# Kernel tuning notes

Measured on AMD Instinct MI355X. Metric: run time of the kernel, lower is better.

Reference implementation:

```python
import jax, jax.numpy as jnp
import numpy as np

N_HEADS = 8
FACTOR = 5


def setup_inputs() -> dict:
    key = jax.random.key(0)
    ks = jax.random.split(key, 8)
    B, L, D = 2, 4096, 512
    sample_k = min(FACTOR * int(np.ceil(np.log(L))), L)  # 45
    inp = {
        "queries": jax.random.normal(ks[0], (B, L, D), jnp.float32),
        "keys": jax.random.normal(ks[1], (B, L, D), jnp.float32),
        "values": jax.random.normal(ks[2], (B, L, D), jnp.float32),
        "Wq": jax.random.normal(ks[3], (D, D), jnp.float32) * 0.02,
        "bq": jnp.zeros((D,), jnp.float32),
        "Wk": jax.random.normal(ks[4], (D, D), jnp.float32) * 0.02,
        "bk": jnp.zeros((D,), jnp.float32),
        "Wv": jax.random.normal(ks[5], (D, D), jnp.float32) * 0.02,
        "bv": jnp.zeros((D,), jnp.float32),
        "index_sample": jax.random.randint(ks[6], (L, sample_k), 0, L, jnp.int32),
    }
    return inp


def reference(queries, keys, values, Wq, bq, Wk, bk, Wv, bv, index_sample):
    b, l_q, d_model = queries.shape
    _, l_k, _ = keys.shape
    h = N_HEADS
    d = d_model // h
    # projections -> [b, h, l, d]
    q = (queries @ Wq + bq).reshape(b, l_q, h, d).transpose(0, 2, 1, 3)
    k = (keys @ Wk + bk).reshape(b, l_k, h, d).transpose(0, 2, 1, 3)
    v = (values @ Wv + bv).reshape(b, l_k, h, d).transpose(0, 2, 1, 3)
    n_top = min(FACTOR * int(np.ceil(np.log(l_q))), l_q)
    # --- prob_qk: sparse sampled QK ---
    # gather sampled keys per query position: [b, h, l_q, sample_k, d]
    k_sample = k[:, :, index_sample, :]
    q_k_sample = jnp.einsum('bhld,bhlsd->bhls', q, k_sample)
    # sparsity measure M(q, K) = max - mean
    m = q_k_sample.max(-1) - q_k_sample.sum(-1) / l_k  # [b, h, l_q]
    _, m_top = jax.lax.top_k(m, n_top)  # [b, h, n_top]
    q_reduce = jnp.take_along_axis(q, m_top[..., None], axis=2)  # [b, h, u, d]
    scores = jnp.einsum('bhud,bhkd->bhuk', q_reduce, k)  # [b, h, u, l_k]
    scale = float(1.0 / np.sqrt(d))
    scores = scores * scale
    # --- causal ProbMask on the selected query rows ---
    causal = jnp.triu(jnp.ones((l_q, l_k), bool), 1)
    mask = causal[m_top]  # [b, h, u, l_k]
    scores = jnp.where(mask, -jnp.inf, scores)
    attn = jax.nn.softmax(scores, axis=-1)
    # --- initial context: causal cumsum of V; scatter updated rows ---
    context = jnp.cumsum(v, axis=2)  # [b, h, l_q, d]
    upd = jnp.einsum('bhuk,bhkd->bhud', attn, v)
    bi = jnp.arange(b)[:, None, None]
    hi = jnp.arange(h)[None, :, None]
    context = context.at[bi, hi, m_top].set(upd)
    return context.transpose(0, 2, 1, 3).reshape(b, l_q, h * d)
```

## Files before the change

kernel.cpp:

```cpp
#include <hip/hip_runtime.h>
#include <math.h>

#define B  2
#define L  4096
#define D  512
#define H  8
#define DH 64
#define BH (B * H)
#define K3 1536
#define XPW 1024

typedef short s16x8 __attribute__((ext_vector_type(8)));
typedef float f32x4 __attribute__((ext_vector_type(4)));

#define AS1 __attribute__((address_space(1)))
#define AS3 __attribute__((address_space(3)))

__device__ __forceinline__ void lds_load16(const void* g, void* l) {
    __builtin_amdgcn_global_load_lds((const AS1 unsigned int*)g,
                                     (AS3 unsigned int*)l, 16, 0, 0);
}

__device__ __forceinline__ unsigned short f2bf(float x) {
    union { float f; unsigned u; } v; v.f = x;
    unsigned u = v.u;
    return (unsigned short)((u + 0x7fff + ((u >> 16) & 1)) >> 16);
}
__device__ __forceinline__ float bf2f(unsigned short h) {
    union { float f; unsigned u; } v; v.u = ((unsigned)h) << 16;
    return v.f;
}

#define MEMFENCE asm volatile("" ::: "memory")
__device__ __forceinline__ void wg_bar() {
    MEMFENCE;
    __builtin_amdgcn_s_barrier();
    MEMFENCE;
}

__global__ __launch_bounds__(256)
void k_split(const float* __restrict__ q, const float* __restrict__ k,
             const float* __restrict__ v,
             const float* __restrict__ wq, const float* __restrict__ wk,
             const float* __restrict__ wv,
             unsigned short* __restrict__ Xp, unsigned short* __restrict__ WpT)
{
    const int tid = threadIdx.x;
    if (blockIdx.x < 192) {
        __shared__ float t[64][65];
        const int bx = blockIdx.x;
        const int e  = bx >> 6;
        const int k0 = (bx & 7) * 64;
        const int n0 = ((bx >> 3) & 7) * 64;
        const float* W = (e == 0) ? wq : (e == 1) ? wk : wv;

        for (int idx = tid; idx < 64 * 16; idx += 256) {
            const int i = idx >> 4, j4 = (idx & 15) << 2;
            *(float4*)&t[i][j4] = *(const float4*)(W + (size_t)(k0 + i) * 512 + n0 + j4);
        }
        __syncthreads();

        const int n_loc = tid >> 2;
        const int kq    = (tid & 3) << 4;
        unsigned short h[16], l[16];
        #pragma unroll
        for (int tt = 0; tt < 16; tt++) {
            const float x = t[kq + tt][n_loc];
            h[tt] = f2bf(x);
            l[tt] = f2bf(x - bf2f(h[tt]));
        }
        unsigned short* base = WpT + (size_t)e * 512 * K3 + (size_t)(n0 + n_loc) * K3 + k0 + kq;
        #pragma unroll
        for (int g4 = 0; g4 < 4; g4++) {
            ushort4 hv = make_ushort4(h[g4*4], h[g4*4+1], h[g4*4+2], h[g4*4+3]);
            ushort4 lv = make_ushort4(l[g4*4], l[g4*4+1], l[g4*4+2], l[g4*4+3]);
            *(ushort4*)(base + g4*4)        = hv;
            *(ushort4*)(base + 512 + g4*4)  = lv;
            *(ushort4*)(base + 1024 + g4*4) = hv;
        }
    } else {
        const size_t g = (size_t)(blockIdx.x - 192) * 256 + tid;
        const size_t per = (size_t)8192 * 128;
        const int e = (int)(g / per);
        const size_t rem = g - (size_t)e * per;
        const int m  = (int)(rem >> 7);
        const int kq = (int)(rem & 127) << 2;

        const float* X = (e == 0) ? q : (e == 1) ? k : v;
        const float4 x = *(const float4*)(X + (size_t)m * 512 + kq);

        unsigned short h0 = f2bf(x.x), h1 = f2bf(x.y), h2 = f2bf(x.z), h3 = f2bf(x.w);
        unsigned short* dst = Xp + (size_t)e * 8192 * XPW + (size_t)m * XPW + kq;
        *(ushort4*)(dst) = make_ushort4(h0, h1, h2, h3);
        if (e != 2) {
            unsigned short l0 = f2bf(x.x - bf2f(h0)), l1 = f2bf(x.y - bf2f(h1));
            unsigned short l2 = f2bf(x.z - bf2f(h2)), l3 = f2bf(x.w - bf2f(h3));
            *(ushort4*)(dst + 512) = make_ushort4(l0, l1, l2, l3);
        }
    }
}

#define MFMA16 __builtin_amdgcn_mfma_f32_16x16x32_bf16

__global__ __launch_bounds__(512, 2)
void gemm_mfma(const unsigned short* __restrict__ Xp,
               const unsigned short* __restrict__ WpT,
               const float* __restrict__ bq, const float* __restrict__ bk,
               const float* __restrict__ bv,
               float* __restrict__ Qo, float* __restrict__ Ko,
               float* __restrict__ Vo)
{
    __shared__ __align__(16) unsigned short lds[65536];

    const int e = blockIdx.z;
    const float* bias = (e == 0) ? bq : (e == 1) ? bk : bv;
    float* C          = (e == 0) ? Qo : (e == 1) ? Ko : Vo;
    const unsigned short* Ag = Xp  + (size_t)e * 8192 * XPW;
    const unsigned short* Bg = WpT + (size_t)e * 512 * K3;
    const int NT = (e == 2) ? 8 : 24;

    const int tid  = threadIdx.x;
    const int lane = tid & 63;
    const int wid  = tid >> 6;
    const int wm   = wid & 1;
    const int wn   = wid >> 1;
    const int m0   = blockIdx.x * 256;
    const int n0g  = blockIdx.y * 256;

    const int srow = wid * 8 + (lane >> 3);
    const int scq8 = ((lane & 7) ^ (lane >> 3)) << 3;
    const unsigned short* aSrc = Ag + (size_t)(m0 + srow) * XPW + scq8;
    const unsigned short* bSrc = Bg + (size_t)(n0g + srow) * K3 + scq8;
    unsigned short* ldsA = lds;
    unsigned short* ldsB = lds + 32768;
    unsigned short* dA = ldsA + wid * 512;
    unsigned short* dB = ldsB + wid * 512;

    const int r16 = lane & 15, quad = lane >> 4;
    const int x3 = r16 & 7;
    const int c0 = ((quad ^ x3) << 4);
    const int c1 = (((4 | quad) ^ x3) << 4);
    const char* fA = (const char*)ldsA + (wm * 128 + r16) * 128;
    const char* fB = (const char*)ldsB + (wn * 64 + r16) * 128;

    f32x4 acc[8][4];
    #pragma unroll
    for (int i = 0; i < 8; i++)
        #pragma unroll
        for (int j = 0; j < 4; j++)
            acc[i][j] = (f32x4){0.f, 0.f, 0.f, 0.f};

    #pragma unroll
    for (int j = 0; j < 4; j++)
        lds_load16(aSrc + (size_t)(j * 64) * XPW, dA + j * 4096);
    #pragma unroll
    for (int j = 0; j < 4; j++)
        lds_load16(bSrc + (size_t)(j * 64) * K3, dB + j * 4096);

    s16x8 aF[8], b0[4], b1[4];

    for (int t = 0; t < NT; ++t) {
        const int pa = (t & 1) << 15;
        const int na = (~t & 1) * 16384;
        if (t + 1 < NT) {
            const int k1 = (t + 1) * 64;
            const int ka = (k1 < 512) ? k1 : k1 - 512;
            #pragma unroll
            for (int j = 0; j < 4; j++)
                lds_load16(aSrc + (size_t)(j * 64) * XPW + ka, dA + na + j * 4096);
            asm volatile("s_waitcnt vmcnt(4)" ::: "memory");
        } else {
            asm volatile("s_waitcnt vmcnt(0)" ::: "memory");
        }
        wg_bar();
        #pragma unroll
        for (int mq = 0; mq < 4; mq++) {
            aF[mq * 2]     = *(const s16x8*)(fA + pa + mq * 2048 + c0);
            aF[mq * 2 + 1] = *(const s16x8*)(fA + pa + mq * 2048 + c1);
        }
        #pragma unroll
        for (int nq = 0; nq < 2; nq++) {
            b0[nq * 2]     = *(const s16x8*)(fB + pa + nq * 2048 + c0);
            b0[nq * 2 + 1] = *(const s16x8*)(fB + pa + nq * 2048 + c1);
        }
        wg_bar();
        asm volatile("s_waitcnt lgkmcnt(0)" ::: "memory");
        __builtin_amdgcn_s_setprio(1);
        #pragma unroll
        for (int mq = 0; mq < 4; mq++)
            #pragma unroll
            for (int nq = 0; nq < 2; nq++) {
                acc[mq][nq] = MFMA16(aF[mq*2],   b0[nq*2],   acc[mq][nq], 0, 0, 0);
                acc[mq][nq] = MFMA16(aF[mq*2+1], b0[nq*2+1], acc[mq][nq], 0, 0, 0);
            }
        __builtin_amdgcn_s_setprio(0);
        wg_bar();
        if (t + 1 < NT) {
            const int kb = (t + 1) * 64;
            #pragma unroll
            for (int j = 0; j < 4; j++)
                lds_load16(bSrc + (size_t)(j * 64) * K3 + kb, dB + na + j * 4096);
        }
        #pragma unroll
        for (int nq = 0; nq < 2; nq++) {
            b1[nq * 2]     = *(const s16x8*)(fB + pa + (2 + nq) * 2048 + c0);
            b1[nq * 2 + 1] = *(const s16x8*)(fB + pa + (2 + nq) * 2048 + c1);
        }
        wg_bar();
        asm volatile("s_waitcnt lgkmcnt(0)" ::: "memory");
        __builtin_amdgcn_s_setprio(1);
        #pragma unroll
        for (int mq = 0; mq < 4; mq++)
            #pragma unroll
            for (int nq = 0; nq < 2; nq++) {
                acc[mq][2+nq] = MFMA16(aF[mq*2],   b1[nq*2],   acc[mq][2+nq], 0, 0, 0);
                acc[mq][2+nq] = MFMA16(aF[mq*2+1], b1[nq*2+1], acc[mq][2+nq], 0, 0, 0);
            }
        __builtin_amdgcn_s_setprio(0);
        wg_bar();
        #pragma unroll
        for (int mq = 0; mq < 4; mq++) {
            aF[mq * 2]     = *(const s16x8*)(fA + pa + 8192 + mq * 2048 + c0);
            aF[mq * 2 + 1] = *(const s16x8*)(fA + pa + 8192 + mq * 2048 + c1);
        }
        wg_bar();
        asm volatile("s_waitcnt lgkmcnt(0)" ::: "memory");
        __builtin_amdgcn_s_setprio(1);
        #pragma unroll
        for (int mq = 0; mq < 4; mq++)
            #pragma unroll
            for (int nq = 0; nq < 2; nq++) {
                acc[4+mq][2+nq] = MFMA16(aF[mq*2],   b1[nq*2],   acc[4+mq][2+nq], 0, 0, 0);
                acc[4+mq][2+nq] = MFMA16(aF[mq*2+1], b1[nq*2+1], acc[4+mq][2+nq], 0, 0, 0);
            }
        __builtin_amdgcn_s_setprio(0);
        wg_bar();
        __builtin_amdgcn_s_setprio(1);
        #pragma unroll
        for (int mq = 0; mq < 4; mq++)
            #pragma unroll
            for (int nq = 0; nq < 2; nq++) {
                acc[4+mq][nq] = MFMA16(aF[mq*2],   b0[nq*2],   acc[4+mq][nq], 0, 0, 0);
                acc[4+mq][nq] = MFMA16(aF[mq*2+1], b0[nq*2+1], acc[4+mq][nq], 0, 0, 0);
            }
        __builtin_amdgcn_s_setprio(0);
        wg_bar();
    }

    #pragma unroll
    for (int nt = 0; nt < 4; nt++) {
        const int col = n0g + wn * 64 + nt * 16 + r16;
        const float bb = bias[col];
        #pragma unroll
        for (int mt = 0; mt < 8; mt++) {
            const int row0 = m0 + wm * 128 + mt * 16 + quad * 4;
            #pragma unroll
            for (int i = 0; i < 4; i++)
                C[(size_t)(row0 + i) * 512 + col] = acc[mt][nt][i] + bb;
        }
    }
}

#define CH 64
__global__ __launch_bounds__(256)
void k_sample_chunks(const float* __restrict__ Q, const float* __restrict__ K,
                     const int* __restrict__ idx, float* __restrict__ m_out, int S,
                     const float* __restrict__ V, float* __restrict__ partial)
{
    const int tid = threadIdx.x;
    if (blockIdx.x < 256) {
        const int bid = blockIdx.x;
        const int c  = (bid & 15) * 4 + (tid >> 6);
        const int h  = (bid >> 4) & (H - 1);
        const int b  = bid >> 7;
        const int d  = tid & 63;
        const float* base = V + (size_t)b * L * D + h * DH + d + (size_t)(c * CH) * D;

        float vals[CH];
        #pragma unroll
        for (int i = 0; i < CH; i++) vals[i] = base[(size_t)i * D];

        float s0 = 0.f, s1 = 0.f, s2 = 0.f, s3 = 0.f;
        #pragma unroll
        for (int i = 0; i < CH; i += 4) {
            s0 += vals[i]; s1 += vals[i+1]; s2 += vals[i+2]; s3 += vals[i+3];
        }
        partial[((size_t)((b * H + h) * 64 + c)) * DH + d] = (s0 + s1) + (s2 + s3);
    } else {
        const int lane = tid & 63;
        const int wib  = tid >> 6;
        const int i    = blockIdx.x - 256;
        const int bh   = i & 15;
        const int lg   = i >> 4;
        const int l = lg * 4 + wib;
        const int h = bh & (H - 1);
        const int b = bh >> 3;
        const int widx = (bh << 12) | l;

        const int r4 = lane >> 2;
        const int c4 = lane & 3;

        float4 qf[4];
        {
            const float4* qv = (const float4*)(Q + ((size_t)b * L + l) * D + h * DH);
            #pragma unroll
            for (int ii = 0; ii < 4; ii++) qf[ii] = qv[c4 + 4 * ii];
        }

        const float* Kb = K + (size_t)b * L * D + h * DH;
        const int* is = idx + (size_t)l * S;

        int  jj[3];
        bool ok[3];
        #pragma unroll
        for (int p = 0; p < 3; p++) {
            const int sp = p * 16 + r4;
            ok[p] = sp < S;
            jj[p] = ok[p] ? is[sp] : 0;
        }
        float4 kv[3][4];
        #pragma unroll
        for (int p = 0; p < 3; p++) {
            const float4* Krow = (const float4*)(Kb + (size_t)jj[p] * D);
            #pragma unroll
            for (int ii = 0; ii < 4; ii++) kv[p][ii] = Krow[c4 + 4 * ii];
        }

        float vmax = -INFINITY, vsum = 0.f;
        #pragma unroll
        for (int p = 0; p < 3; p++) {
            float dot = 0.f;
            #pragma unroll
            for (int ii = 0; ii < 4; ii++) {
                const float4 kvv = kv[p][ii];
                const float4 qq = qf[ii];
                dot += qq.x * kvv.x + qq.y * kvv.y + qq.z * kvv.z + qq.w * kvv.w;
            }
            dot += __shfl_xor(dot, 1, 64);
            dot += __shfl_xor(dot, 2, 64);
            if (ok[p]) {
                vmax = fmaxf(vmax, dot);
                if (c4 == 0) vsum += dot;
            }
        }
        #pragma unroll
        for (int off = 32; off >= 4; off >>= 1) {
            vmax = fmaxf(vmax, __shfl_xor(vmax, off, 64));
            vsum += __shfl_xor(vsum, off, 64);
        }
        if (lane == 0) m_out[widx] = vmax - vsum * (1.0f / (float)L);
    }
}

__global__ __launch_bounds__(256)
void topk_kernel(const float* __restrict__ m_in, int* __restrict__ m_top,
                 float* __restrict__ sums, int* __restrict__ flags, int NT)
{
    __shared__ unsigned hist[256];
    __shared__ unsigned sfx[257];
    __shared__ int sh_b, sh_rem;
    __shared__ int cnt_gt, cnt_eq;
    __shared__ int eqlist[128];

    const float* m = m_in + (size_t)blockIdx.x * L;
    const int tid = threadIdx.x;
    int* out = m_top + blockIdx.x * NT;
    int* fl  = flags + (size_t)blockIdx.x * L;

    if (tid < NT) sums[blockIdx.x * NT + tid] = 0.f;
    for (int i = tid; i < L; i += 256) fl[i] = 0;

    unsigned uv[16];
    #pragma unroll
    for (int k = 0; k < 16; k++) {
        const float f = m[tid + k * 256];
        const unsigned x = __float_as_uint(f);
        uv[k] = (x & 0x80000000u) ? ~x : (x | 0x80000000u);
    }

    unsigned prefix = 0;
    int rem = NT;

    for (int level = 0; level < 4; level++) {
        const int shift = 24 - level * 8;
        hist[tid] = 0;
        if (tid == 0) { cnt_gt = 0; cnt_eq = 0; }
        __syncthreads();
        #pragma unroll
        for (int k = 0; k < 16; k++) {
            const bool part = (level == 0) || ((uv[k] >> (shift + 8)) == prefix);
            if (part) atomicAdd(&hist[(uv[k] >> shift) & 255], 1u);
        }
        __syncthreads();
        if (tid < 64) {
            const unsigned s0 = hist[4*tid+0], s1 = hist[4*tid+1];
            const unsigned s2 = hist[4*tid+2], s3 = hist[4*tid+3];
            const unsigned loc = s0 + s1 + s2 + s3;
            unsigned suf = loc;
            #pragma unroll
            for (int off = 1; off < 64; off <<= 1) {
                const unsigned t = __shfl_down(suf, off, 64);
                if (tid + off < 64) suf += t;
            }
            const unsigned tail = suf - loc;
            sfx[4*tid+3] = tail + s3;
            sfx[4*tid+2] = tail + s3 + s2;
            sfx[4*tid+1] = tail + s3 + s2 + s1;
            sfx[4*tid+0] = suf;
            if (tid == 0) sfx[256] = 0;
        }
        __syncthreads();
        if (sfx[tid + 1] < (unsigned)rem && (unsigned)rem <= sfx[tid]) {
            sh_b   = tid;
            sh_rem = rem - (int)sfx[tid + 1];
        }
        __syncthreads();
        prefix = (prefix << 8) | (unsigned)sh_b;
        rem    = sh_rem;
        __syncthreads();
    }

    const unsigned T = prefix;
    const int n_gt = NT - rem;

    #pragma unroll
    for (int k = 0; k < 16; k++) {
        if (uv[k] > T) {
            const int pos = atomicAdd(&cnt_gt, 1);
            out[pos] = tid + k * 256;
        } else if (uv[k] == T) {
            const int pos = atomicAdd(&cnt_eq, 1);
            if (pos < 128) eqlist[pos] = tid + k * 256;
        }
    }
    __syncthreads();
    if (tid == 0) {
        int n = cnt_eq < 128 ? cnt_eq : 128;
        for (int r = 0; r < rem; r++) {
            int best = 0x7fffffff, bi = 0;
            for (int i = 0; i < n; i++)
                if (eqlist[i] < best) { best = eqlist[i]; bi = i; }
            out[n_gt + r] = best;
            eqlist[bi] = 0x7fffffff;
        }
    }
    __syncthreads();
    if (tid < NT) fl[out[tid]] = 1;
}

__global__ __launch_bounds__(256)
void k_cumsum_scores(const float* __restrict__ V, const float* __restrict__ partial,
                     const int* __restrict__ flags, float* __restrict__ out,
                     const float* __restrict__ Q, const float* __restrict__ K,
                     const int* __restrict__ m_top, float* __restrict__ scores,
                     float* __restrict__ sums, int NT)
{
    const int tid = threadIdx.x;
    if (blockIdx.x < 256) {
        const int bid = blockIdx.x;
        const int c  = (bid & 15) * 4 + (tid >> 6);
        const int h  = (bid >> 4) & (H - 1);
        const int b  = bid >> 7;
        const int d  = tid & 63;
        const size_t off = (size_t)b * L * D + h * DH + d + (size_t)(c * CH) * D;
        const float* base  = V   + off;
        float*       obase = out + off;
        const float* pb = partial + (size_t)((b * H + h) * 64) * DH + d;
        const int*   fp = flags + (size_t)(b * H + h) * L + c * CH;

        float vals[CH];
        #pragma unroll
        for (int i = 0; i < CH; i++) vals[i] = base[(size_t)i * D];

        float acc = 0.f;
        for (int cc = 0; cc < c; cc++) acc += pb[cc * DH];

        #pragma unroll
        for (int i = 0; i < CH; i++) {
            acc += vals[i];
            obase[(size_t)i * D] = fp[i] ? 0.f : acc;
        }
    } else {
        __shared__ float qsh[15][DH];
        __shared__ int   psh[15];

        const int rem2 = blockIdx.x - 256;
        const int bh = rem2 / 24;
        const int r2 = rem2 % 24;
        const int ug = r2 >> 3;
        const int jc = r2 & 7;
        const int h  = bh & (H - 1);
        const int b  = bh >> 3;
        const int j0 = jc * 512;

        for (int i = tid; i < 15 * DH; i += 256) {
            const int u = i >> 6, d = i & 63;
            const int p = m_top[bh * NT + ug * 15 + u];
            if (d == 0) psh[u] = p;
            qsh[u][d] = Q[((size_t)b * L + p) * D + h * DH + d];
        }
        __syncthreads();

        const float* Kb = K + (size_t)b * L * D + h * DH;
        const int ja = j0 + tid;
        const int jb = ja + 256;
        float4 k0[16], k1[16];
        {
            const float4* ra = (const float4*)(Kb + (size_t)ja * D);
            const float4* rb = (const float4*)(Kb + (size_t)jb * D);
            #pragma unroll
            for (int i = 0; i < 16; i++) { k0[i] = ra[i]; k1[i] = rb[i]; }
        }

        for (int u = 0; u < 15; u++) {
            const int p = psh[u];
            const float4* qv = (const float4*)qsh[u];
            float d0 = 0.f, d1 = 0.f;
            #pragma unroll
            for (int i = 0; i < 16; i++) {
                const float4 q4 = qv[i];
                d0 += q4.x * k0[i].x + q4.y * k0[i].y + q4.z * k0[i].z + q4.w * k0[i].w;
                d1 += q4.x * k1[i].x + q4.y * k1[i].y + q4.z * k1[i].z + q4.w * k1[i].w;
            }
            const float e0 = (ja <= p) ? __expf(d0 * 0.125f) : 0.f;
            const float e1 = (jb <= p) ? __expf(d1 * 0.125f) : 0.f;
            float* srow = scores + (size_t)(bh * NT + ug * 15 + u) * L;
            srow[ja] = e0;
            srow[jb] = e1;
            float t = e0 + e1;
            #pragma unroll
            for (int off = 32; off; off >>= 1) t += __shfl_xor(t, off, 64);
            if ((tid & 63) == 0) atomicAdd(&sums[bh * NT + ug * 15 + u], t);
        }
    }
}

__global__ __launch_bounds__(256)
void attn_wv(const float* __restrict__ scores, const float* __restrict__ V,
             const int* __restrict__ m_top, const float* __restrict__ sums,
             float* __restrict__ out, int NT)
{
    __shared__ float ssh[45][64];
    __shared__ float sinv[45];
    __shared__ int   psh[45];

    const int bh = blockIdx.y;
    const int h  = bh & (H - 1);
    const int b  = bh >> 3;
    const int j0 = blockIdx.x * 64;
    const int tid = threadIdx.x;
    const int d   = tid & 63;
    const int w   = tid >> 6;

    if (tid < NT) {
        psh[tid]  = m_top[bh * NT + tid];
        sinv[tid] = 1.0f / sums[bh * NT + tid];
    }

    const float* Vb = V + (size_t)b * L * D + h * DH + d;
    float vreg[64];
    #pragma unroll
    for (int i = 0; i < 64; i++) vreg[i] = Vb[(size_t)(j0 + i) * D];

    __syncthreads();
    for (int i = tid; i < NT * 64; i += 256) {
        const int u = i >> 6, j = i & 63;
        ssh[u][j] = scores[(size_t)(bh * NT + u) * L + j0 + j] * sinv[u];
    }
    __syncthreads();

    for (int u = w; u < NT; u += 4) {
        const int p = psh[u];
        if (p < j0) continue;
        const float* wt = ssh[u];
        float acc = 0.f;
        #pragma unroll
        for (int i = 0; i < 64; i++) acc += wt[i] * vreg[i];
        atomicAdd(out + ((size_t)b * L + p) * D + h * DH + d, acc);
    }
}

extern "C" void kernel_launch(void* const* d_in, const int* in_sizes, int n_in,
                              void* d_out, int out_size, void* d_ws, size_t ws_size,
                              hipStream_t stream)
{
    const float* queries = (const float*)d_in[0];
    const float* keys    = (const float*)d_in[1];
    const float* values  = (const float*)d_in[2];
    const float* Wq      = (const float*)d_in[3];
    const float* bq      = (const float*)d_in[4];
    const float* Wk      = (const float*)d_in[5];
    const float* bk      = (const float*)d_in[6];
    const float* Wv      = (const float*)d_in[7];
    const float* bv      = (const float*)d_in[8];
    const int*   idx     = (const int*)d_in[9];
    float* out = (float*)d_out;

    const int S  = in_sizes[9] / L;
    const int NT = S;

    const size_t NE = (size_t)B * L * D;
    float* Qb      = (float*)d_ws;
    float* Kb      = Qb + NE;
    float* Vb      = Kb + NE;
    float* m_buf   = Vb + NE;
    float* cs_part = m_buf + (size_t)BH * L;
    int*   m_top   = (int*)(cs_part + (size_t)BH * 64 * DH);
    float* sums    = (float*)(m_top + 1024);
    int*   flags   = (int*)(sums + 1024);
    float* scores  = (float*)(flags + (size_t)BH * L);
    unsigned short* Xp  = (unsigned short*)(scores + (size_t)BH * NT * L);
    unsigned short* WpT = Xp + (size_t)3 * 8192 * XPW;

    k_split<<<192 + 3 * 8192 * 128 / 256, 256, 0, stream>>>(
        queries, keys, values, Wq, Wk, Wv, Xp, WpT);

    gemm_mfma<<<dim3(8192 / 256, 512 / 256, 3), 512, 0, stream>>>(
        Xp, WpT, bq, bk, bv, Qb, Kb, Vb);

    k_sample_chunks<<<256 + BH * L / 4, 256, 0, stream>>>(
        Qb, Kb, idx, m_buf, S, Vb, cs_part);

    topk_kernel<<<BH, 256, 0, stream>>>(m_buf, m_top, sums, flags, NT);

    k_cumsum_scores<<<256 + 384, 256, 0, stream>>>(
        Vb, cs_part, flags, out, Qb, Kb, m_top, scores, sums, NT);

    attn_wv<<<dim3(64, BH), 256, 0, stream>>>(scores, Vb, m_top, sums, out, NT);
}
```

Baseline: 262.7 us.

## Split-K the Q/K projection GEMMs into three partial products with atomic accumulation

The Q and K projections compute three bf16 partial products (hi*hi, hi*lo, lo*hi). These were a single 24-step K loop per block. They now run as three separate 8-step grid slices (grid z=7) that atomically add into output buffers, which the split kernel first fills with the bias. This raises the GEMM's block count from 192 to 448 so more CUs are busy. The cost is extra global atomic traffic, an extra bias-initialisation pass, and summation order that is no longer deterministic.

```diff
diff --git a/kernel.cpp b/kernel.cpp
--- a/kernel.cpp
+++ b/kernel.cpp
@@ -43,7 +43,9 @@
              const float* __restrict__ v,
              const float* __restrict__ wq, const float* __restrict__ wk,
              const float* __restrict__ wv,
-             unsigned short* __restrict__ Xp, unsigned short* __restrict__ WpT)
+             unsigned short* __restrict__ Xp, unsigned short* __restrict__ WpT,
+             float* __restrict__ Qb, float* __restrict__ Kb,
+             const float* __restrict__ bq, const float* __restrict__ bk)
 {
     const int tid = threadIdx.x;
     if (blockIdx.x < 192) {
@@ -78,7 +80,7 @@
             *(ushort4*)(base + 512 + g4*4)  = lv;
             *(ushort4*)(base + 1024 + g4*4) = hv;
         }
-    } else {
+    } else if (blockIdx.x < 192 + 12288) {
         const size_t g = (size_t)(blockIdx.x - 192) * 256 + tid;
         const size_t per = (size_t)8192 * 128;
         const int e = (int)(g / per);
@@ -97,6 +99,22 @@
             unsigned short l2 = f2bf(x.z - bf2f(h2)), l3 = f2bf(x.w - bf2f(h3));
             *(ushort4*)(dst + 512) = make_ushort4(l0, l1, l2, l3);
         }
+    } else {
+        const int gi = blockIdx.x - (192 + 12288);
+        const size_t li = (size_t)gi * 4096 + (size_t)tid * 16;
+        const size_t NEh = (size_t)8192 * 512;
+        float* buf; const float* bias; size_t w;
+        if (li < NEh) { buf = Qb; bias = bq; w = li; }
+        else          { buf = Kb; bias = bk; w = li - NEh; }
+        const int n = (int)(w & 511);
+        const float4 b0 = *(const float4*)(bias + n);
+        const float4 b1 = *(const float4*)(bias + n + 4);
+        const float4 b2 = *(const float4*)(bias + n + 8);
+        const float4 b3 = *(const float4*)(bias + n + 12);
+        *(float4*)(buf + w)      = b0;
+        *(float4*)(buf + w + 4)  = b1;
+        *(float4*)(buf + w + 8)  = b2;
+        *(float4*)(buf + w + 12) = b3;
     }
 }
 
@@ -112,12 +130,14 @@
 {
     __shared__ __align__(16) unsigned short lds[65536];
 
-    const int e = blockIdx.z;
+    const int z = blockIdx.z;
+    const int e = z / 3;
+    const int s = z % 3;
     const float* bias = (e == 0) ? bq : (e == 1) ? bk : bv;
     float* C          = (e == 0) ? Qo : (e == 1) ? Ko : Vo;
-    const unsigned short* Ag = Xp  + (size_t)e * 8192 * XPW;
-    const unsigned short* Bg = WpT + (size_t)e * 512 * K3;
-    const int NT = (e == 2) ? 8 : 24;
+    const unsigned short* Ag = Xp  + (size_t)e * 8192 * XPW + (s == 2 ? 512 : 0);
+    const unsigned short* Bg = WpT + (size_t)e * 512 * K3 + s * 512;
+    const int NT = 8;
 
     const int tid  = threadIdx.x;
     const int lane = tid & 63;
@@ -163,8 +183,7 @@
         const int pa = (t & 1) << 15;
         const int na = (~t & 1) * 16384;
         if (t + 1 < NT) {
-            const int k1 = (t + 1) * 64;
-            const int ka = (k1 < 512) ? k1 : k1 - 512;
+            const int ka = (t + 1) * 64;
             #pragma unroll
             for (int j = 0; j < 4; j++)
                 lds_load16(aSrc + (size_t)(j * 64) * XPW + ka, dA + na + j * 4096);
@@ -247,16 +266,30 @@
         wg_bar();
     }
 
-    #pragma unroll
-    for (int nt = 0; nt < 4; nt++) {
-        const int col = n0g + wn * 64 + nt * 16 + r16;
-        const float bb = bias[col];
-        #pragma unroll
-        for (int mt = 0; mt < 8; mt++) {
-            const int row0 = m0 + wm * 128 + mt * 16 + quad * 4;
-            #pragma unroll
-            for (int i = 0; i < 4; i++)
-                C[(size_t)(row0 + i) * 512 + col] = acc[mt][nt][i] + bb;
+    if (e == 2) {
+        #pragma unroll
+        for (int nt = 0; nt < 4; nt++) {
+            const int col = n0g + wn * 64 + nt * 16 + r16;
+            const float bb = bias[col];
+            #pragma unroll
+            for (int mt = 0; mt < 8; mt++) {
+                const int row0 = m0 + wm * 128 + mt * 16 + quad * 4;
+                #pragma unroll
+                for (int i = 0; i < 4; i++)
+                    C[(size_t)(row0 + i) * 512 + col] = acc[mt][nt][i] + bb;
+            }
+        }
+    } else {
+        #pragma unroll
+        for (int nt = 0; nt < 4; nt++) {
+            const int col = n0g + wn * 64 + nt * 16 + r16;
+            #pragma unroll
+            for (int mt = 0; mt < 8; mt++) {
+                const int row0 = m0 + wm * 128 + mt * 16 + quad * 4;
+                #pragma unroll
+                for (int i = 0; i < 4; i++)
+                    atomicAdd(&C[(size_t)(row0 + i) * 512 + col], acc[mt][nt][i]);
+            }
         }
     }
 }
@@ -612,10 +645,10 @@
     unsigned short* Xp  = (unsigned short*)(scores + (size_t)BH * NT * L);
     unsigned short* WpT = Xp + (size_t)3 * 8192 * XPW;
 
-    k_split<<<192 + 3 * 8192 * 128 / 256, 256, 0, stream>>>(
-        queries, keys, values, Wq, Wk, Wv, Xp, WpT);
-
-    gemm_mfma<<<dim3(8192 / 256, 512 / 256, 3), 512, 0, stream>>>(
+    k_split<<<192 + 3 * 8192 * 128 / 256 + 2048, 256, 0, stream>>>(
+        queries, keys, values, Wq, Wk, Wv, Xp, WpT, Qb, Kb, bq, bk);
+
+    gemm_mfma<<<dim3(8192 / 256, 512 / 256, 7), 512, 0, stream>>>(
         Xp, WpT, bq, bk, bv, Qb, Kb, Vb);
 
     k_sample_chunks<<<256 + BH * L / 4, 256, 0, stream>>>(
```

Result: slower. 329.7 us (+25.5%).

## Prefetch A and B tiles together and cut barriers in projection GEMM loop

Applied to the files above, without the earlier changes.

In the bf16 MFMA projection GEMM, the next B tile is now prefetched into LDS together with the next A tile at the top of each k-iteration, waiting with vmcnt(8). The inner MFMA phases are merged into two larger blocks that each cover both halves of the N dimension. The intermediate workgroup barriers and explicit lgkmcnt waits are removed, leaving one barrier before the LDS reads and one at the end of the iteration. The aim is to cut synchronisation overhead and give the scheduler longer MFMA runs, at the cost of less interleaving of global loads with compute and longer register live ranges for the B fragments.

```diff
diff --git a/kernel.cpp b/kernel.cpp
--- a/kernel.cpp
+++ b/kernel.cpp
@@ -162,17 +162,22 @@
     for (int t = 0; t < NT; ++t) {
         const int pa = (t & 1) << 15;
         const int na = (~t & 1) * 16384;
+
         if (t + 1 < NT) {
             const int k1 = (t + 1) * 64;
             const int ka = (k1 < 512) ? k1 : k1 - 512;
             #pragma unroll
             for (int j = 0; j < 4; j++)
                 lds_load16(aSrc + (size_t)(j * 64) * XPW + ka, dA + na + j * 4096);
-            asm volatile("s_waitcnt vmcnt(4)" ::: "memory");
+            #pragma unroll
+            for (int j = 0; j < 4; j++)
+                lds_load16(bSrc + (size_t)(j * 64) * K3 + k1, dB + na + j * 4096);
+            asm volatile("s_waitcnt vmcnt(8)" ::: "memory");
         } else {
             asm volatile("s_waitcnt vmcnt(0)" ::: "memory");
         }
         wg_bar();
+
         #pragma unroll
         for (int mq = 0; mq < 4; mq++) {
             aF[mq * 2]     = *(const s16x8*)(fA + pa + mq * 2048 + c0);
@@ -182,66 +187,35 @@
         for (int nq = 0; nq < 2; nq++) {
             b0[nq * 2]     = *(const s16x8*)(fB + pa + nq * 2048 + c0);
             b0[nq * 2 + 1] = *(const s16x8*)(fB + pa + nq * 2048 + c1);
-        }
-        wg_bar();
-        asm volatile("s_waitcnt lgkmcnt(0)" ::: "memory");
-        __builtin_amdgcn_s_setprio(1);
-        #pragma unroll
-        for (int mq = 0; mq < 4; mq++)
-            #pragma unroll
-            for (int nq = 0; nq < 2; nq++) {
-                acc[mq][nq] = MFMA16(aF[mq*2],   b0[nq*2],   acc[mq][nq], 0, 0, 0);
-                acc[mq][nq] = MFMA16(aF[mq*2+1], b0[nq*2+1], acc[mq][nq], 0, 0, 0);
-            }
-        __builtin_amdgcn_s_setprio(0);
-        wg_bar();
-        if (t + 1 < NT) {
-            const int kb = (t + 1) * 64;
-            #pragma unroll
-            for (int j = 0; j < 4; j++)
-                lds_load16(bSrc + (size_t)(j * 64) * K3 + kb, dB + na + j * 4096);
-        }
-        #pragma unroll
-        for (int nq = 0; nq < 2; nq++) {
             b1[nq * 2]     = *(const s16x8*)(fB + pa + (2 + nq) * 2048 + c0);
             b1[nq * 2 + 1] = *(const s16x8*)(fB + pa + (2 + nq) * 2048 + c1);
         }
-        wg_bar();
-        asm volatile("s_waitcnt lgkmcnt(0)" ::: "memory");
         __builtin_amdgcn_s_setprio(1);
         #pragma unroll
         for (int mq = 0; mq < 4; mq++)
             #pragma unroll
             for (int nq = 0; nq < 2; nq++) {
+                acc[mq][nq]   = MFMA16(aF[mq*2],   b0[nq*2],   acc[mq][nq],   0, 0, 0);
+                acc[mq][nq]   = MFMA16(aF[mq*2+1], b0[nq*2+1], acc[mq][nq],   0, 0, 0);
                 acc[mq][2+nq] = MFMA16(aF[mq*2],   b1[nq*2],   acc[mq][2+nq], 0, 0, 0);
                 acc[mq][2+nq] = MFMA16(aF[mq*2+1], b1[nq*2+1], acc[mq][2+nq], 0, 0, 0);
             }
         __builtin_amdgcn_s_setprio(0);
-        wg_bar();
+
         #pragma unroll
         for (int mq = 0; mq < 4; mq++) {
             aF[mq * 2]     = *(const s16x8*)(fA + pa + 8192 + mq * 2048 + c0);
             aF[mq * 2 + 1] = *(const s16x8*)(fA + pa + 8192 + mq * 2048 + c1);
         }
-        wg_bar();
-        asm volatile("s_waitcnt lgkmcnt(0)" ::: "memory");
         __builtin_amdgcn_s_setprio(1);
         #pragma unroll
         for (int mq = 0; mq < 4; mq++)
             #pragma unroll
             for (int nq = 0; nq < 2; nq++) {
+                acc[4+mq][nq]   = MFMA16(aF[mq*2],   b0[nq*2],   acc[4+mq][nq],   0, 0, 0);
+                acc[4+mq][nq]   = MFMA16(aF[mq*2+1], b0[nq*2+1], acc[4+mq][nq],   0, 0, 0);
                 acc[4+mq][2+nq] = MFMA16(aF[mq*2],   b1[nq*2],   acc[4+mq][2+nq], 0, 0, 0);
                 acc[4+mq][2+nq] = MFMA16(aF[mq*2+1], b1[nq*2+1], acc[4+mq][2+nq], 0, 0, 0);
-            }
-        __builtin_amdgcn_s_setprio(0);
-        wg_bar();
-        __builtin_amdgcn_s_setprio(1);
-        #pragma unroll
-        for (int mq = 0; mq < 4; mq++)
-            #pragma unroll
-            for (int nq = 0; nq < 2; nq++) {
-                acc[4+mq][nq] = MFMA16(aF[mq*2],   b0[nq*2],   acc[4+mq][nq], 0, 0, 0);
-                acc[4+mq][nq] = MFMA16(aF[mq*2+1], b0[nq*2+1], acc[4+mq][nq], 0, 0, 0);
             }
         __builtin_amdgcn_s_setprio(0);
         wg_bar();
```

Result: no change. 266.7 us (+1.5%).
